# Optimization experiments

Hardware: AMD Instinct MI355X
Metric: run time of the kernel (lower is better)

The kernel has to match this reference:

```python
import jax, jax.numpy as jnp
import numpy as np

N_MODULES = 8
AG_HIDDEN = 512
N_HID = 512
OUT_SIZE = 10
BATCH = 8192


def _state_mask(n_modules, n0, n1):
    # torch: eye(M).repeat_interleave(n0, 0).repeat_interleave(n1, 1)
    m = jnp.eye(n_modules, dtype=jnp.float32)
    return jnp.repeat(jnp.repeat(m, n0, axis=0), n1, axis=1)


def setup_inputs() -> dict:
    key = jax.random.key(0)
    ks = jax.random.split(key, 5)
    d_in = N_MODULES * AG_HIDDEN
    d_hid = N_MODULES * N_HID
    d_out = N_MODULES * OUT_SIZE
    s1 = 1.0 / np.sqrt(d_in)
    s2 = 1.0 / np.sqrt(d_hid)
    return {
        "x": jax.random.normal(ks[0], (BATCH, d_in), jnp.float32),
        "W1": jax.random.uniform(ks[1], (d_hid, d_in), jnp.float32, -s1, s1),
        "b1": jax.random.uniform(ks[2], (d_hid,), jnp.float32, -s1, s1),
        "W2": jax.random.uniform(ks[3], (d_out, d_hid), jnp.float32, -s2, s2),
        "b2": jax.random.uniform(ks[4], (d_out,), jnp.float32, -s2, s2),
    }


def reference(x, W1, b1, W2, b2):
    # block-diagonal masks (intra-module connectivity only)
    mask1 = _state_mask(N_MODULES, N_HID, AG_HIDDEN)   # [d_hid, d_in]
    mask2 = _state_mask(N_MODULES, OUT_SIZE, N_HID)    # [d_out, d_hid]
    h = jax.nn.relu(x @ (W1 * mask1).T + b1)           # [B, d_hid]
    y = h @ (W2 * mask2).T + b2                        # [B, d_out]
    # split(OUT_SIZE, -1) then stack on dim 1 == reshape to [B, n_modules, OUT_SIZE]
    return y.reshape(y.shape[0], N_MODULES, OUT_SIZE)
```

## Files before the change

### kernel.cpp

```cpp
#include <hip/hip_runtime.h>


#define NMOD 8
#define DIM 512
#define OSZ 10
#define BATCH 8192
#define D_IN 4096
#define D_OUT 80
#define BM 128
#define BN 256
#define BK 32
#define NK (DIM / BK)

#define ASTRIDE 40
#define HSTRIDE 264
#define A_SZ 5120
#define B_SZ 8192

#define LDSA_SZ 5120
#define LDSB_SZ 8192

#define VMCNT(n) asm volatile("s_waitcnt vmcnt(" #n ")" ::: "memory")
#define LGKM0()  asm volatile("s_waitcnt lgkmcnt(0)" ::: "memory")
#define MEMFENCE() asm volatile("" ::: "memory")

typedef __attribute__((ext_vector_type(8))) short short8;
typedef __attribute__((ext_vector_type(4))) float float4v;
typedef __attribute__((ext_vector_type(4))) unsigned int uint4v;

__device__ __forceinline__ unsigned short f2bf(float f) {
    unsigned int u = __builtin_bit_cast(unsigned int, f);
    u += 0x7fffu + ((u >> 16) & 1u);
    return (unsigned short)(u >> 16);
}

__device__ __forceinline__ unsigned int pk2(float a, float b) {
    unsigned int r;
    asm("v_cvt_pk_bf16_f32 %0, %1, %2" : "=v"(r) : "v"(a), "v"(b));
    return r;
}

__device__ __forceinline__ short8 cvt8(float4 a, float4 b) {
    uint4v u = {pk2(a.x, a.y), pk2(a.z, a.w), pk2(b.x, b.y), pk2(b.z, b.w)};
    return __builtin_bit_cast(short8, u);
}

__global__ void init_out_kernel(const float* __restrict__ b2, float* __restrict__ out) {
    int idx = blockIdx.x * 256 + threadIdx.x;
    out[idx] = b2[idx % D_OUT];
}

__global__ void cvt_w_kernel(const float* __restrict__ W1, ushort* __restrict__ w1b) {
    int j = blockIdx.x * 256 + threadIdx.x;
    int mm = j >> 16, rem = j & 65535, r = rem >> 7, c4 = rem & 127;
    float4 v = *(const float4*)(W1 + (size_t)(mm * DIM + r) * D_IN + mm * DIM + c4 * 4);
    *(ushort4*)(w1b + (size_t)mm * DIM * DIM + r * DIM + c4 * 4) =
        make_ushort4(f2bf(v.x), f2bf(v.y), f2bf(v.z), f2bf(v.w));
}

__global__ __launch_bounds__(256, 2)
void fused_pipe(const float* __restrict__ x, const ushort* __restrict__ w1b,
                const float* __restrict__ b1, const float* __restrict__ W2,
                float* __restrict__ out) {
    __shared__ __attribute__((aligned(16))) ushort smem[26624];
    ushort* A0 = smem;
    ushort* A1 = smem + A_SZ;
    ushort* B0 = smem + 2 * A_SZ;
    ushort* B1 = smem + 2 * A_SZ + B_SZ;
    ushort* ldsH = smem;

    const int tid  = threadIdx.x;
    const int wave = tid >> 6;
    const int lane = tid & 63;
    const int r16  = lane & 15;
    const int kq   = lane >> 4;

    const int bid     = blockIdx.x;
    const int m       = bid & 7;
    const int half    = (bid >> 3) & 1;
    const int rowBase = (bid >> 4) * BM;

    const float*  xsrc = x + (size_t)rowBase * D_IN + m * DIM;
    const ushort* w1h  = w1b + (size_t)m * DIM * DIM + (size_t)half * BN * DIM;

    const int arow = tid >> 1;
    const int ah   = tid & 1;
    const int bl4  = lane >> 2;
    const int bc   = lane & 3;

    float4v acc[8][4];
#pragma unroll
    for (int i = 0; i < 8; i++)
#pragma unroll
        for (int j = 0; j < 4; j++) acc[i][j] = (float4v){0.f, 0.f, 0.f, 0.f};

    float4 xrA[4], xrB[4];

    auto issueX = [&](int k, float4 (&xr)[4]) {
        const float* p = xsrc + (size_t)arow * D_IN + k * BK + ah * 16;
        xr[0] = *(const float4*)p;       xr[1] = *(const float4*)(p + 4);
        xr[2] = *(const float4*)(p + 8); xr[3] = *(const float4*)(p + 12);
    };
    auto issueW = [&](int k, ushort* Bn) {
#pragma unroll
        for (int r = 0; r < 4; r++) {
            const int row = wave * 64 + r * 16 + bl4;
            const int f   = (row >> 1) & 3;
            __builtin_amdgcn_global_load_lds(
                (const __attribute__((address_space(1))) void*)(w1h + (size_t)row * DIM + k * BK + (bc ^ f) * 8),
                (__attribute__((address_space(3))) void*)(Bn + row * BK + bc * 8), 16, 0, 0);
        }
    };
    auto writeA = [&](float4 (&xr)[4], ushort* An) {
        *(short8*)(An + arow * ASTRIDE + ah * 16)     = cvt8(xr[0], xr[1]);
        *(short8*)(An + arow * ASTRIDE + ah * 16 + 8) = cvt8(xr[2], xr[3]);
    };

    short8 aF[8], bF[4];
    auto readA = [&](const ushort* Ac) {
#pragma unroll
        for (int mt = 0; mt < 8; mt++)
            aF[mt] = *(const short8*)(Ac + (mt * 16 + r16) * ASTRIDE + kq * 8);
    };
    auto readB = [&](const ushort* Bc) {
#pragma unroll
        for (int nt = 0; nt < 4; nt++) {
            const int row = wave * 64 + nt * 16 + r16;
            bF[nt] = *(const short8*)(Bc + row * BK + (kq ^ ((row >> 1) & 3)) * 8);
        }
    };
    auto mfma = [&]() {
#pragma unroll
        for (int mt = 0; mt < 8; mt++)
#pragma unroll
            for (int nt = 0; nt < 4; nt++)
                acc[mt][nt] = __builtin_amdgcn_mfma_f32_16x16x32_bf16(aF[mt], bF[nt], acc[mt][nt], 0, 0, 0);
    };

    issueX(0, xrA);  MEMFENCE();
    issueW(0, B0);   MEMFENCE();
    issueX(1, xrB);  MEMFENCE();
    issueW(1, B1);
    VMCNT(12);
    writeA(xrA, A0);
    LGKM0();
    __builtin_amdgcn_s_barrier();
    MEMFENCE();

#define STEADY_ITER(KP2, Ac, Bc, An, XRD, XRI)                                 \
    do {                                                                       \
        issueX((KP2), (XRI)); MEMFENCE();                                      \
        readA((Ac));                                                           \
        VMCNT(12);                                                             \
        readB((Bc));                                                           \
        LGKM0();                                                               \
        issueW((KP2), (Bc)); MEMFENCE();                                       \
        mfma();                                                                \
        MEMFENCE();                                                            \
        VMCNT(12);                                                             \
        writeA((XRD), (An));                                                   \
        LGKM0();                                                               \
        __builtin_amdgcn_s_barrier();                                          \
        MEMFENCE();                                                            \
    } while (0)

    for (int k2 = 0; k2 < 14; k2 += 2) {
        STEADY_ITER(k2 + 2, A0, B0, A1, xrB, xrA);
        STEADY_ITER(k2 + 3, A1, B1, A0, xrA, xrB);
    }
#undef STEADY_ITER
    {
        readA(A0);
        VMCNT(8);
        readB(B0);
        LGKM0();
        mfma();
        MEMFENCE();
        VMCNT(4);
        writeA(xrB, A1);
        LGKM0();
        __builtin_amdgcn_s_barrier();
        MEMFENCE();
    }
    {
        readA(A1);
        VMCNT(0);
        readB(B1);
        LGKM0();
        mfma();
        MEMFENCE();
    }

    float b1v[4];
#pragma unroll
    for (int nt = 0; nt < 4; nt++)
        b1v[nt] = b1[m * DIM + half * BN + wave * 64 + nt * 16 + r16];

    for (int hh = 0; hh < 2; hh++) {
        __syncthreads();
#pragma unroll
        for (int mt2 = 0; mt2 < 4; mt2++) {
            const int mt = hh * 4 + mt2;
#pragma unroll
            for (int nt = 0; nt < 4; nt++) {
#pragma unroll
                for (int reg = 0; reg < 4; reg++) {
                    float v = acc[mt][nt][reg] + b1v[nt];
                    v = v > 0.f ? v : 0.f;
                    const int lr  = mt2 * 16 + kq * 4 + reg;
                    const int col = wave * 64 + nt * 16 + r16;
                    ldsH[lr * HSTRIDE + col] = f2bf(v);
                }
            }
        }
        __syncthreads();

        {
            float4v acc2 = (float4v){0.f, 0.f, 0.f, 0.f};
            const int hrow = wave * 16 + r16;
            const float* w2row = W2 + (size_t)(m * OSZ + r16) * D_IN + m * DIM + half * BN;
#pragma unroll
            for (int kc = 0; kc < BN / 32; kc++) {
                const int c = kc * 32 + kq * 8;
                short8 hA = *(const short8*)(ldsH + hrow * HSTRIDE + c);
                short8 wb = {0, 0, 0, 0, 0, 0, 0, 0};
                if (r16 < OSZ) {
                    const float* p = w2row + c;
                    wb = cvt8(*(const float4*)p, *(const float4*)(p + 4));
                }
                acc2 = __builtin_amdgcn_mfma_f32_16x16x32_bf16(hA, wb, acc2, 0, 0, 0);
            }
            if (r16 < OSZ) {
#pragma unroll
                for (int reg = 0; reg < 4; reg++) {
                    const int grow = rowBase + hh * 64 + wave * 16 + kq * 4 + reg;
                    atomicAdd(out + (size_t)grow * D_OUT + m * OSZ + r16, acc2[reg]);
                }
            }
        }
    }
}

__global__ __launch_bounds__(256, 2)
void fused_kernel(const float* __restrict__ x, const float* __restrict__ W1,
                  const float* __restrict__ b1, const float* __restrict__ W2,
                  float* __restrict__ out) {
    __shared__ __attribute__((aligned(16))) ushort smem[26624];
    ushort* ldsA0 = smem;
    ushort* ldsA1 = smem + LDSA_SZ;
    ushort* ldsB0 = smem + 2 * LDSA_SZ;
    ushort* ldsB1 = smem + 2 * LDSA_SZ + LDSB_SZ;
    ushort* ldsH  = smem;

    const int tid  = threadIdx.x;
    const int wave = tid >> 6;
    const int lane = tid & 63;
    const int r16  = lane & 15;
    const int kq   = lane >> 4;

    const int bid     = blockIdx.x;
    const int m       = bid & 7;
    const int half    = (bid >> 3) & 1;
    const int rowBase = (bid >> 4) * BM;

    const float*  xsrc = x + (size_t)rowBase * D_IN + m * DIM;
    const float*  w1f  = W1 + (size_t)(m * DIM + half * BN) * D_IN + m * DIM;

    const int arow = tid >> 1;
    const int ah   = tid & 1;
    const int brow = tid >> 2;
    const int bc   = tid & 3;

    float4v acc[8][4];
#pragma unroll
    for (int i = 0; i < 8; i++)
#pragma unroll
        for (int j = 0; j < 4; j++) acc[i][j] = (float4v){0.f, 0.f, 0.f, 0.f};

#pragma unroll
    for (int r = 0; r < 4; r++) {
        const int row = r * 64 + brow;
        const int f   = (row >> 1) & 3;
        const float* p = w1f + (size_t)row * D_IN + bc * 8;
        *(short8*)(ldsB0 + row * BK + (bc ^ f) * 8) = cvt8(*(const float4*)p, *(const float4*)(p + 4));
    }
    {
        const float* p = xsrc + (size_t)arow * D_IN + ah * 16;
        float4 a0 = *(const float4*)p, a1 = *(const float4*)(p + 4);
        float4 a2 = *(const float4*)(p + 8), a3 = *(const float4*)(p + 12);
        *(short8*)(ldsA0 + arow * ASTRIDE + ah * 16)     = cvt8(a0, a1);
        *(short8*)(ldsA0 + arow * ASTRIDE + ah * 16 + 8) = cvt8(a2, a3);
    }

    for (int kk = 0; kk < NK; kk++) {
        __syncthreads();
        ushort* Ac = (kk & 1) ? ldsA1 : ldsA0;
        ushort* Bc = (kk & 1) ? ldsB1 : ldsB0;
        ushort* An = (kk & 1) ? ldsA0 : ldsA1;
        ushort* Bn = (kk & 1) ? ldsB0 : ldsB1;

        float4 xr0, xr1, xr2, xr3;
        const bool pf = (kk < NK - 1);
        if (pf) {
            const float* p = xsrc + (size_t)arow * D_IN + kk * BK + BK + ah * 16;
            xr0 = *(const float4*)p;     xr1 = *(const float4*)(p + 4);
            xr2 = *(const float4*)(p + 8); xr3 = *(const float4*)(p + 12);
        }

        short8 aF[8], bF[4];
#pragma unroll
        for (int mt = 0; mt < 8; mt++)
            aF[mt] = *(const short8*)(Ac + (mt * 16 + r16) * ASTRIDE + kq * 8);
#pragma unroll
        for (int nt = 0; nt < 4; nt++) {
            const int row = wave * 64 + nt * 16 + r16;
            bF[nt] = *(const short8*)(Bc + row * BK + (kq ^ ((row >> 1) & 3)) * 8);
        }
#pragma unroll
        for (int mt = 0; mt < 8; mt++)
#pragma unroll
            for (int nt = 0; nt < 4; nt++)
                acc[mt][nt] = __builtin_amdgcn_mfma_f32_16x16x32_bf16(aF[mt], bF[nt], acc[mt][nt], 0, 0, 0);

        if (pf) {
            *(short8*)(An + arow * ASTRIDE + ah * 16)     = cvt8(xr0, xr1);
            *(short8*)(An + arow * ASTRIDE + ah * 16 + 8) = cvt8(xr2, xr3);
#pragma unroll
            for (int r = 0; r < 4; r++) {
                const int row = r * 64 + brow;
                const int f   = (row >> 1) & 3;
                const float* p = w1f + (size_t)row * D_IN + kk * BK + BK + bc * 8;
                *(short8*)(Bn + row * BK + (bc ^ f) * 8) = cvt8(*(const float4*)p, *(const float4*)(p + 4));
            }
        }
    }

    float b1v[4];
#pragma unroll
    for (int nt = 0; nt < 4; nt++)
        b1v[nt] = b1[m * DIM + half * BN + wave * 64 + nt * 16 + r16];

    for (int hh = 0; hh < 2; hh++) {
        __syncthreads();
#pragma unroll
        for (int mt2 = 0; mt2 < 4; mt2++) {
            const int mt = hh * 4 + mt2;
#pragma unroll
            for (int nt = 0; nt < 4; nt++) {
#pragma unroll
                for (int reg = 0; reg < 4; reg++) {
                    float v = acc[mt][nt][reg] + b1v[nt];
                    v = v > 0.f ? v : 0.f;
                    const int lr  = mt2 * 16 + kq * 4 + reg;
                    const int col = wave * 64 + nt * 16 + r16;
                    ldsH[lr * HSTRIDE + col] = f2bf(v);
                }
            }
        }
        __syncthreads();

        {
            float4v acc2 = (float4v){0.f, 0.f, 0.f, 0.f};
            const int hrow = wave * 16 + r16;
            const float* w2row = W2 + (size_t)(m * OSZ + r16) * D_IN + m * DIM + half * BN;
#pragma unroll
            for (int kc = 0; kc < BN / 32; kc++) {
                const int c = kc * 32 + kq * 8;
                short8 hA = *(const short8*)(ldsH + hrow * HSTRIDE + c);
                short8 wb = {0, 0, 0, 0, 0, 0, 0, 0};
                if (r16 < OSZ) {
                    const float* p = w2row + c;
                    wb = cvt8(*(const float4*)p, *(const float4*)(p + 4));
                }
                acc2 = __builtin_amdgcn_mfma_f32_16x16x32_bf16(hA, wb, acc2, 0, 0, 0);
            }
            if (r16 < OSZ) {
#pragma unroll
                for (int reg = 0; reg < 4; reg++) {
                    const int grow = rowBase + hh * 64 + wave * 16 + kq * 4 + reg;
                    atomicAdd(out + (size_t)grow * D_OUT + m * OSZ + r16, acc2[reg]);
                }
            }
        }
    }
}

extern "C" void kernel_launch(void* const* d_in, const int* in_sizes, int n_in,
                              void* d_out, int out_size, void* d_ws, size_t ws_size,
                              hipStream_t stream) {
    const float* x  = (const float*)d_in[0];
    const float* W1 = (const float*)d_in[1];
    const float* b1 = (const float*)d_in[2];
    const float* W2 = (const float*)d_in[3];
    const float* b2 = (const float*)d_in[4];
    float* out = (float*)d_out;

    init_out_kernel<<<dim3(2560), dim3(256), 0, stream>>>(b2, out);

    if (ws_size >= (size_t)NMOD * DIM * DIM * sizeof(ushort)) {
        ushort* w1b = (ushort*)d_ws;
        cvt_w_kernel<<<dim3(2048), dim3(256), 0, stream>>>(W1, w1b);
        fused_pipe<<<dim3(1024), dim3(256), 0, stream>>>(x, w1b, b1, W2, out);
    } else {
        fused_kernel<<<dim3(1024), dim3(256), 0, stream>>>(x, W1, b1, W2, out);
    }
}
```

Baseline: 257.0 us.

## Pre-convert x to MFMA-fragment bf16 layout and compute full hidden per block

Adds a pre-pass that converts x to bf16 and stores it in an MFMA-fragment-ordered layout, so the main kernel loads A fragments straight from global memory into registers with no LDS staging. The main kernel becomes a 512-thread block covering the full 512-wide hidden dimension of one module. That removes the half split and the atomicAdd reduction: the bias b2 is added and outputs are written directly, and the init kernel is dropped. The costs are an extra full pass over x (read fp32, write bf16), a larger workspace requirement, and higher register pressure from double-buffered A fragments.

```diff
diff --git a/kernel.cpp b/kernel.cpp
--- a/kernel.cpp
+++ b/kernel.cpp
@@ -8,20 +8,20 @@
 #define D_IN 4096
 #define D_OUT 80
 #define BM 128
-#define BN 256
 #define BK 32
 #define NK (DIM / BK)
 
+#define B_ROWS 512
+#define B_SZ (B_ROWS * BK)
+#define XB_SHORTS ((size_t)BATCH * D_IN)
+#define XGRAN (BATCH * D_IN / 8)
+
+#define LDSA_SZ 5120
+#define LDSB_SZ 8192
 #define ASTRIDE 40
 #define HSTRIDE 264
-#define A_SZ 5120
-#define B_SZ 8192
-
-#define LDSA_SZ 5120
-#define LDSB_SZ 8192
 
 #define VMCNT(n) asm volatile("s_waitcnt vmcnt(" #n ")" ::: "memory")
-#define LGKM0()  asm volatile("s_waitcnt lgkmcnt(0)" ::: "memory")
 #define MEMFENCE() asm volatile("" ::: "memory")
 
 typedef __attribute__((ext_vector_type(8))) short short8;
@@ -48,6 +48,16 @@
 __global__ void init_out_kernel(const float* __restrict__ b2, float* __restrict__ out) {
     int idx = blockIdx.x * 256 + threadIdx.x;
     out[idx] = b2[idx % D_OUT];
+}
+
+__global__ void cvt_x_kernel(const float* __restrict__ x, ushort* __restrict__ xb) {
+    int j = blockIdx.x * 256 + threadIdx.x;
+    int row = j >> 9, k8 = j & 511;
+    const float* p = x + (size_t)row * D_IN + k8 * 8;
+    int m = k8 >> 6, kmod = k8 & 63, kk = kmod >> 2, kq = kmod & 3;
+    int tile = row >> 7, mt = (row >> 4) & 7, r16 = row & 15;
+    size_t g = ((size_t)(((m * 64 + tile) * 16 + kk) * 8 + mt) << 6) + kq * 16 + r16;
+    *(short8*)(xb + g * 8) = cvt8(*(const float4*)p, *(const float4*)(p + 4));
 }
 
 __global__ void cvt_w_kernel(const float* __restrict__ W1, ushort* __restrict__ w1b) {
@@ -58,15 +68,13 @@
         make_ushort4(f2bf(v.x), f2bf(v.y), f2bf(v.z), f2bf(v.w));
 }
 
-__global__ __launch_bounds__(256, 2)
-void fused_pipe(const float* __restrict__ x, const ushort* __restrict__ w1b,
-                const float* __restrict__ b1, const float* __restrict__ W2,
-                float* __restrict__ out) {
-    __shared__ __attribute__((aligned(16))) ushort smem[26624];
-    ushort* A0 = smem;
-    ushort* A1 = smem + A_SZ;
-    ushort* B0 = smem + 2 * A_SZ;
-    ushort* B1 = smem + 2 * A_SZ + B_SZ;
+__global__ __launch_bounds__(512, 4)
+void fused_full2(const ushort* __restrict__ xb, const ushort* __restrict__ w1b,
+                 const float* __restrict__ b1, const float* __restrict__ W2,
+                 const float* __restrict__ b2, float* __restrict__ out) {
+    __shared__ __attribute__((aligned(16))) ushort smem[32768];
+    ushort* B0 = smem;
+    ushort* B1 = smem + B_SZ;
     ushort* ldsH = smem;
 
     const int tid  = threadIdx.x;
@@ -77,16 +85,14 @@
 
     const int bid     = blockIdx.x;
     const int m       = bid & 7;
-    const int half    = (bid >> 3) & 1;
-    const int rowBase = (bid >> 4) * BM;
-
-    const float*  xsrc = x + (size_t)rowBase * D_IN + m * DIM;
-    const ushort* w1h  = w1b + (size_t)m * DIM * DIM + (size_t)half * BN * DIM;
-
-    const int arow = tid >> 1;
-    const int ah   = tid & 1;
-    const int bl4  = lane >> 2;
-    const int bc   = lane & 3;
+    const int tile    = bid >> 3;
+    const int rowBase = tile * BM;
+
+    const ushort* w1m = w1b + (size_t)m * DIM * DIM;
+    const ushort* xfb = xb + ((size_t)(m * 64 + tile) << 16) + lane * 8;
+
+    const int brow = tid >> 2;
+    const int bc   = tid & 3;
 
     float4v acc[8][4];
 #pragma unroll
@@ -94,33 +100,23 @@
 #pragma unroll
         for (int j = 0; j < 4; j++) acc[i][j] = (float4v){0.f, 0.f, 0.f, 0.f};
 
-    float4 xrA[4], xrB[4];
-
-    auto issueX = [&](int k, float4 (&xr)[4]) {
-        const float* p = xsrc + (size_t)arow * D_IN + k * BK + ah * 16;
-        xr[0] = *(const float4*)p;       xr[1] = *(const float4*)(p + 4);
-        xr[2] = *(const float4*)(p + 8); xr[3] = *(const float4*)(p + 12);
-    };
+    short8 aC[8], aN[8], bF[4];
+
     auto issueW = [&](int k, ushort* Bn) {
 #pragma unroll
         for (int r = 0; r < 4; r++) {
-            const int row = wave * 64 + r * 16 + bl4;
+            const int row = r * 128 + brow;
             const int f   = (row >> 1) & 3;
             __builtin_amdgcn_global_load_lds(
-                (const __attribute__((address_space(1))) void*)(w1h + (size_t)row * DIM + k * BK + (bc ^ f) * 8),
+                (const __attribute__((address_space(1))) void*)(w1m + (size_t)row * DIM + k * BK + (bc ^ f) * 8),
                 (__attribute__((address_space(3))) void*)(Bn + row * BK + bc * 8), 16, 0, 0);
         }
     };
-    auto writeA = [&](float4 (&xr)[4], ushort* An) {
-        *(short8*)(An + arow * ASTRIDE + ah * 16)     = cvt8(xr[0], xr[1]);
-        *(short8*)(An + arow * ASTRIDE + ah * 16 + 8) = cvt8(xr[2], xr[3]);
-    };
-
-    short8 aF[8], bF[4];
-    auto readA = [&](const ushort* Ac) {
+    auto issueA = [&](int kk, short8 (&a)[8]) {
+        const ushort* p = xfb + kk * 4096;
 #pragma unroll
         for (int mt = 0; mt < 8; mt++)
-            aF[mt] = *(const short8*)(Ac + (mt * 16 + r16) * ASTRIDE + kq * 8);
+            a[mt] = *(const short8*)(p + mt * 512);
     };
     auto readB = [&](const ushort* Bc) {
 #pragma unroll
@@ -129,73 +125,64 @@
             bF[nt] = *(const short8*)(Bc + row * BK + (kq ^ ((row >> 1) & 3)) * 8);
         }
     };
-    auto mfma = [&]() {
+    auto mfma = [&](short8 (&a)[8]) {
 #pragma unroll
         for (int mt = 0; mt < 8; mt++)
 #pragma unroll
             for (int nt = 0; nt < 4; nt++)
-                acc[mt][nt] = __builtin_amdgcn_mfma_f32_16x16x32_bf16(aF[mt], bF[nt], acc[mt][nt], 0, 0, 0);
+                acc[mt][nt] = __builtin_amdgcn_mfma_f32_16x16x32_bf16(a[mt], bF[nt], acc[mt][nt], 0, 0, 0);
     };
 
-    issueX(0, xrA);  MEMFENCE();
     issueW(0, B0);   MEMFENCE();
-    issueX(1, xrB);  MEMFENCE();
-    issueW(1, B1);
-    VMCNT(12);
-    writeA(xrA, A0);
-    LGKM0();
+    issueA(0, aC);
+    VMCNT(8);
     __builtin_amdgcn_s_barrier();
     MEMFENCE();
 
-#define STEADY_ITER(KP2, Ac, Bc, An, XRD, XRI)                                 \
-    do {                                                                       \
-        issueX((KP2), (XRI)); MEMFENCE();                                      \
-        readA((Ac));                                                           \
-        VMCNT(12);                                                             \
-        readB((Bc));                                                           \
-        LGKM0();                                                               \
-        issueW((KP2), (Bc)); MEMFENCE();                                       \
-        mfma();                                                                \
-        MEMFENCE();                                                            \
-        VMCNT(12);                                                             \
-        writeA((XRD), (An));                                                   \
-        LGKM0();                                                               \
-        __builtin_amdgcn_s_barrier();                                          \
-        MEMFENCE();                                                            \
-    } while (0)
-
     for (int k2 = 0; k2 < 14; k2 += 2) {
-        STEADY_ITER(k2 + 2, A0, B0, A1, xrB, xrA);
-        STEADY_ITER(k2 + 3, A1, B1, A0, xrA, xrB);
-    }
-#undef STEADY_ITER
+        {
+            issueW(k2 + 1, B1); MEMFENCE();
+            issueA(k2 + 1, aN); MEMFENCE();
+            readB(B0);
+            mfma(aC);
+            MEMFENCE();
+            VMCNT(8);
+            __builtin_amdgcn_s_barrier();
+            MEMFENCE();
+        }
+        {
+            issueW(k2 + 2, B0); MEMFENCE();
+            issueA(k2 + 2, aC); MEMFENCE();
+            readB(B1);
+            mfma(aN);
+            MEMFENCE();
+            VMCNT(8);
+            __builtin_amdgcn_s_barrier();
+            MEMFENCE();
+        }
+    }
     {
-        readA(A0);
+        issueW(15, B1); MEMFENCE();
+        issueA(15, aN); MEMFENCE();
+        readB(B0);
+        mfma(aC);
+        MEMFENCE();
         VMCNT(8);
-        readB(B0);
-        LGKM0();
-        mfma();
-        MEMFENCE();
-        VMCNT(4);
-        writeA(xrB, A1);
-        LGKM0();
         __builtin_amdgcn_s_barrier();
         MEMFENCE();
     }
     {
-        readA(A1);
-        VMCNT(0);
         readB(B1);
-        LGKM0();
-        mfma();
+        mfma(aN);
         MEMFENCE();
     }
 
     float b1v[4];
 #pragma unroll
     for (int nt = 0; nt < 4; nt++)
-        b1v[nt] = b1[m * DIM + half * BN + wave * 64 + nt * 16 + r16];
-
+        b1v[nt] = b1[m * DIM + wave * 64 + nt * 16 + r16];
+
+    const float b2v = (r16 < OSZ) ? b2[m * OSZ + r16] : 0.f;
     for (int hh = 0; hh < 2; hh++) {
         __syncthreads();
 #pragma unroll
@@ -209,23 +196,24 @@
                     v = v > 0.f ? v : 0.f;
                     const int lr  = mt2 * 16 + kq * 4 + reg;
                     const int col = wave * 64 + nt * 16 + r16;
-                    ldsH[lr * HSTRIDE + col] = f2bf(v);
-                }
-            }
-        }
-        __syncthreads();
-
-        {
+                    const int g = col >> 3, c7 = col & 7;
+                    ldsH[lr * 512 + ((g ^ ((reg & 1) << 2)) << 3) + c7] = f2bf(v);
+                }
+            }
+        }
+        __syncthreads();
+
+        if (wave < 4) {
             float4v acc2 = (float4v){0.f, 0.f, 0.f, 0.f};
-            const int hrow = wave * 16 + r16;
-            const float* w2row = W2 + (size_t)(m * OSZ + r16) * D_IN + m * DIM + half * BN;
-#pragma unroll
-            for (int kc = 0; kc < BN / 32; kc++) {
-                const int c = kc * 32 + kq * 8;
-                short8 hA = *(const short8*)(ldsH + hrow * HSTRIDE + c);
+            const float* w2row = W2 + (size_t)(m * OSZ + r16) * D_IN + m * DIM;
+#pragma unroll
+            for (int kc = 0; kc < 16; kc++) {
+                const int hrow = wave * 16 + r16;
+                const int slot = (kc * 4 + kq) ^ ((r16 & 1) << 2);
+                short8 hA = *(const short8*)(ldsH + hrow * 512 + slot * 8);
                 short8 wb = {0, 0, 0, 0, 0, 0, 0, 0};
                 if (r16 < OSZ) {
-                    const float* p = w2row + c;
+                    const float* p = w2row + kc * 32 + kq * 8;
                     wb = cvt8(*(const float4*)p, *(const float4*)(p + 4));
                 }
                 acc2 = __builtin_amdgcn_mfma_f32_16x16x32_bf16(hA, wb, acc2, 0, 0, 0);
@@ -234,7 +222,7 @@
 #pragma unroll
                 for (int reg = 0; reg < 4; reg++) {
                     const int grow = rowBase + hh * 64 + wave * 16 + kq * 4 + reg;
-                    atomicAdd(out + (size_t)grow * D_OUT + m * OSZ + r16, acc2[reg]);
+                    out[(size_t)grow * D_OUT + m * OSZ + r16] = acc2[reg] + b2v;
                 }
             }
         }
@@ -264,7 +252,7 @@
     const int rowBase = (bid >> 4) * BM;
 
     const float*  xsrc = x + (size_t)rowBase * D_IN + m * DIM;
-    const float*  w1f  = W1 + (size_t)(m * DIM + half * BN) * D_IN + m * DIM;
+    const float*  w1f  = W1 + (size_t)(m * DIM + half * 256) * D_IN + m * DIM;
 
     const int arow = tid >> 1;
     const int ah   = tid & 1;
@@ -338,7 +326,7 @@
     float b1v[4];
 #pragma unroll
     for (int nt = 0; nt < 4; nt++)
-        b1v[nt] = b1[m * DIM + half * BN + wave * 64 + nt * 16 + r16];
+        b1v[nt] = b1[m * DIM + half * 256 + wave * 64 + nt * 16 + r16];
 
     for (int hh = 0; hh < 2; hh++) {
         __syncthreads();
@@ -362,9 +350,9 @@
         {
             float4v acc2 = (float4v){0.f, 0.f, 0.f, 0.f};
             const int hrow = wave * 16 + r16;
-            const float* w2row = W2 + (size_t)(m * OSZ + r16) * D_IN + m * DIM + half * BN;
-#pragma unroll
-            for (int kc = 0; kc < BN / 32; kc++) {
+            const float* w2row = W2 + (size_t)(m * OSZ + r16) * D_IN + m * DIM + half * 256;
+#pragma unroll
+            for (int kc = 0; kc < 8; kc++) {
                 const int c = kc * 32 + kq * 8;
                 short8 hA = *(const short8*)(ldsH + hrow * HSTRIDE + c);
                 short8 wb = {0, 0, 0, 0, 0, 0, 0, 0};
@@ -395,13 +383,16 @@
     const float* b2 = (const float*)d_in[4];
     float* out = (float*)d_out;
 
-    init_out_kernel<<<dim3(2560), dim3(256), 0, stream>>>(b2, out);
-
-    if (ws_size >= (size_t)NMOD * DIM * DIM * sizeof(ushort)) {
-        ushort* w1b = (ushort*)d_ws;
+    const size_t need = XB_SHORTS * sizeof(ushort) +
+                        (size_t)NMOD * DIM * DIM * sizeof(ushort);
+    if (ws_size >= need) {
+        ushort* xb  = (ushort*)d_ws;
+        ushort* w1b = xb + XB_SHORTS;
+        cvt_x_kernel<<<dim3(XGRAN / 256), dim3(256), 0, stream>>>(x, xb);
         cvt_w_kernel<<<dim3(2048), dim3(256), 0, stream>>>(W1, w1b);
-        fused_pipe<<<dim3(1024), dim3(256), 0, stream>>>(x, w1b, b1, W2, out);
+        fused_full2<<<dim3(512), dim3(512), 0, stream>>>(xb, w1b, b1, W2, b2, out);
     } else {
+        init_out_kernel<<<dim3(2560), dim3(256), 0, stream>>>(b2, out);
         fused_kernel<<<dim3(1024), dim3(256), 0, stream>>>(x, W1, b1, W2, out);
     }
 }
```

Result: slower. 803.6 us (+212.7%).
